# Kernel tuning notes

Hardware: AMD Instinct MI355X
Metric: run time of the kernel (lower is better)

The kernel has to match this reference:

```python
import jax, jax.numpy as jnp
import numpy as np

EPS = 1e-6          # VN leaky-relu denominator eps (vn_layers.py)
NEG_SLOPE = 0.2     # VNLinearLeakyReLU default negative_slope
K = 3               # pointops.interpolation default k
DIST_EPS = 1e-8     # interpolation inverse-distance eps


def vn_linear_leakyrelu(x, w_feat, w_dir):
    # x: [B, Cin, 3, N]; w_*: [Cout, Cin]  (bias-free Linears over channel dim)
    p = jnp.einsum('oc,bcvn->bovn', w_feat, x)
    d = jnp.einsum('oc,bcvn->bovn', w_dir, x)
    dot = jnp.sum(p * d, axis=2, keepdims=True)          # [B,Cout,1,N]
    d2 = jnp.sum(d * d, axis=2, keepdims=True)
    mask = (dot >= 0).astype(x.dtype)
    proj = p - (dot / (d2 + EPS)) * d                    # reflect negative part onto plane perp to d
    return NEG_SLOPE * p + (1.0 - NEG_SLOPE) * (mask * p + (1.0 - mask) * proj)


def interpolation(p2, p1, feat, b, n2, n1):
    # p2: [b*n2,3] coarse coords, p1: [b*n1,3] fine coords, feat: [C,3,b*n2]
    # k-NN inverse-squared-distance interpolation, segment-local per cloud.
    C = feat.shape[0]
    p2b = p2.reshape(b, n2, 3)
    p1b = p1.reshape(b, n1, 3)
    featb = feat.reshape(C * 3, b, n2).transpose(1, 2, 0)  # [b, n2, C*3]

    def per_batch(q, s, f):
        d2 = jnp.sum((q[:, None, :] - s[None, :, :]) ** 2, axis=-1)  # [n1,n2]
        neg_d2, idx = jax.lax.top_k(-d2, K)                          # k smallest sq-dists
        w = 1.0 / (-neg_d2 + DIST_EPS)
        w = w / jnp.sum(w, axis=1, keepdims=True)                    # [n1,K]
        return jnp.einsum('nk,nkc->nc', w, f[idx])                   # [n1, C*3]

    out = jax.vmap(per_batch)(p1b, p2b, featb)                       # [b, n1, C*3]
    return out.reshape(b, n1, C, 3).transpose(2, 3, 0, 1).reshape(C, 3, b * n1)


def setup_inputs() -> dict:
    key = jax.random.key(0)
    ks = jax.random.split(key, 8)
    b, n1, n2 = 4, 16384, 4096
    in_planes, out_planes = 128, 64
    p1 = jax.random.uniform(ks[0], (b * n1, 3), dtype=jnp.float32)
    p2 = jax.random.uniform(ks[1], (b * n2, 3), dtype=jnp.float32)
    x1 = jax.random.normal(ks[2], (1, out_planes, 3, b * n1), dtype=jnp.float32)
    x2 = jax.random.normal(ks[3], (1, in_planes, 3, b * n2), dtype=jnp.float32)
    o1 = (jnp.arange(1, b + 1, dtype=jnp.int32)) * n1   # cumulative offsets
    o2 = (jnp.arange(1, b + 1, dtype=jnp.int32)) * n2
    s1 = 1.0 / np.sqrt(out_planes)
    s2 = 1.0 / np.sqrt(in_planes)
    w1_feat = jax.random.uniform(ks[4], (out_planes, out_planes), jnp.float32, -s1, s1)
    w1_dir = jax.random.uniform(ks[5], (out_planes, out_planes), jnp.float32, -s1, s1)
    w2_feat = jax.random.uniform(ks[6], (out_planes, in_planes), jnp.float32, -s2, s2)
    w2_dir = jax.random.uniform(ks[7], (out_planes, in_planes), jnp.float32, -s2, s2)
    return {"p1": p1, "x1": x1, "o1": o1, "p2": p2, "x2": x2, "o2": o2,
            "w1_feat": w1_feat, "w1_dir": w1_dir, "w2_feat": w2_feat, "w2_dir": w2_dir}


def reference(p1, x1, o1, p2, x2, o2, w1_feat, w1_dir, w2_feat, w2_dir):
    b = o1.shape[0]
    n1 = x1.shape[-1] // b
    n2 = x2.shape[-1] // b
    y1 = vn_linear_leakyrelu(x1, w1_feat, w1_dir)            # [1,Cout,3,N1]
    y2 = vn_linear_leakyrelu(x2, w2_feat, w2_dir)[0]         # squeeze(0) -> [Cout,3,N2]
    up = interpolation(p2, p1, y2, b, n2, n1)                # [Cout,3,N1]
    return y1 + up
```

## Files before the change

### kernel.cpp

```cpp
#include <hip/hip_runtime.h>

#define N1T 65536
#define N2T 16384
#define COUT 64
#define CH 192
#define GRD 8
#define HCELL 0.125f

typedef unsigned short bhalf;
typedef __attribute__((ext_vector_type(8))) short short8;
typedef __attribute__((ext_vector_type(4))) float f32x4;

__device__ __forceinline__ bhalf f2bf(float f) {
    unsigned u = __float_as_uint(f);
    return (bhalf)((u + 0x7FFFu + ((u >> 16) & 1u)) >> 16);
}
__device__ __forceinline__ float bf2f(bhalf h) {
    return __uint_as_float(((unsigned)h) << 16);
}

__global__ __launch_bounds__(256) void wconv_kernel(
    const float* __restrict__ w1f, const float* __restrict__ w1d,
    const float* __restrict__ w2f, const float* __restrict__ w2d,
    bhalf* __restrict__ o1fh, bhalf* __restrict__ o1fl,
    bhalf* __restrict__ o1dh, bhalf* __restrict__ o1dl,
    bhalf* __restrict__ o2fh, bhalf* __restrict__ o2fl,
    bhalf* __restrict__ o2dh, bhalf* __restrict__ o2dl) {
    const int i = blockIdx.x * 256 + threadIdx.x;
    if (i < 4096) {
        const float a = w1f[i]; const bhalf ah = f2bf(a);
        o1fh[i] = ah; o1fl[i] = f2bf(a - bf2f(ah));
        const float b = w1d[i]; const bhalf bh = f2bf(b);
        o1dh[i] = bh; o1dl[i] = f2bf(b - bf2f(bh));
    }
    const float a = w2f[i]; const bhalf ah = f2bf(a);
    o2fh[i] = ah; o2fl[i] = f2bf(a - bf2f(ah));
    const float b = w2d[i]; const bhalf bh = f2bf(b);
    o2dh[i] = bh; o2dl[i] = f2bf(b - bf2f(bh));
}

template<int CIN, int N, bool CM>
__global__ __launch_bounds__(256) void vn_mfma_kernel(
    const float* __restrict__ x,
    const bhalf* __restrict__ wfh, const bhalf* __restrict__ wfl,
    const bhalf* __restrict__ wdh, const bhalf* __restrict__ wdl,
    float* __restrict__ out)
{
    constexpr int ROWS = CIN * 3;
    constexpr int LDSC = CIN * 3 + 8;
    __shared__ __align__(16) bhalf xs_h[32][LDSC];
    __shared__ __align__(16) bhalf xs_l[32][LDSC];

    const int tid  = threadIdx.x;
    const int lane = tid & 63;
    const int wave = tid >> 6;
    const int n0   = blockIdx.x * 32;
    const int r16  = lane & 15;
    const int hh   = lane >> 4;
    const int ot   = wave;

    constexpr int NF4 = ROWS * 8;
    for (int i4 = tid; i4 < NF4; i4 += 256) {
        const int row = i4 >> 3, p4 = i4 & 7;
        const float4 v = *(const float4*)&x[(size_t)row * N + n0 + p4 * 4];
        const int c = row / 3, vv = row - c * 3;
        const int col = vv * CIN + c;
        const float vals[4] = {v.x, v.y, v.z, v.w};
#pragma unroll
        for (int j = 0; j < 4; ++j) {
            const bhalf h = f2bf(vals[j]);
            xs_h[p4*4+j][col] = h;
            xs_l[p4*4+j][col] = f2bf(vals[j] - bf2f(h));
        }
    }
    __syncthreads();

    const f32x4 zero = {0.f, 0.f, 0.f, 0.f};
    f32x4 accP[2][3], accD[2][3];
#pragma unroll
    for (int s = 0; s < 2; ++s)
#pragma unroll
        for (int v = 0; v < 3; ++v) { accP[s][v] = zero; accD[s][v] = zero; }

    const int wofs = (ot * 16 + r16) * CIN + hh * 8;
    const bhalf* __restrict__ pfh = wfh + wofs;
    const bhalf* __restrict__ pfl = wfl + wofs;
    const bhalf* __restrict__ pdh = wdh + wofs;
    const bhalf* __restrict__ pdl = wdl + wofs;

#pragma unroll
    for (int k = 0; k < CIN / 32; ++k) {
        const short8 afh = *(const short8*)(pfh + k * 32);
        const short8 afl = *(const short8*)(pfl + k * 32);
        const short8 adh = *(const short8*)(pdh + k * 32);
        const short8 adl = *(const short8*)(pdl + k * 32);
#pragma unroll
        for (int s = 0; s < 2; ++s) {
            const int pt = s * 16 + r16;
#pragma unroll
            for (int v = 0; v < 3; ++v) {
                const short8 bh = *(const short8*)&xs_h[pt][v * CIN + k * 32 + hh * 8];
                const short8 bl = *(const short8*)&xs_l[pt][v * CIN + k * 32 + hh * 8];
                accP[s][v] = __builtin_amdgcn_mfma_f32_16x16x32_bf16(afh, bh, accP[s][v], 0, 0, 0);
                accP[s][v] = __builtin_amdgcn_mfma_f32_16x16x32_bf16(afl, bh, accP[s][v], 0, 0, 0);
                accP[s][v] = __builtin_amdgcn_mfma_f32_16x16x32_bf16(afh, bl, accP[s][v], 0, 0, 0);
                accD[s][v] = __builtin_amdgcn_mfma_f32_16x16x32_bf16(adh, bh, accD[s][v], 0, 0, 0);
                accD[s][v] = __builtin_amdgcn_mfma_f32_16x16x32_bf16(adl, bh, accD[s][v], 0, 0, 0);
                accD[s][v] = __builtin_amdgcn_mfma_f32_16x16x32_bf16(adh, bl, accD[s][v], 0, 0, 0);
            }
        }
    }

    float rr[2][12];
#pragma unroll
    for (int s = 0; s < 2; ++s)
#pragma unroll
        for (int reg = 0; reg < 4; ++reg) {
            const float p0 = accP[s][0][reg], p1 = accP[s][1][reg], p2 = accP[s][2][reg];
            const float q0 = accD[s][0][reg], q1 = accD[s][1][reg], q2 = accD[s][2][reg];
            const float dot = p0*q0 + p1*q1 + p2*q2;
            const float dd  = q0*q0 + q1*q1 + q2*q2;
            const float coef = (dot < 0.f) ? (0.8f * dot / (dd + 1e-6f)) : 0.f;
            rr[s][reg*3+0] = p0 - coef * q0;
            rr[s][reg*3+1] = p1 - coef * q1;
            rr[s][reg*3+2] = p2 - coef * q2;
        }

    if constexpr (!CM) {
#pragma unroll
        for (int s = 0; s < 2; ++s) {
            const int n = n0 + s * 16 + r16;
            float* op = out + (size_t)n * CH + ot * 48 + hh * 12;
            *(float4*)&op[0] = make_float4(rr[s][0], rr[s][1], rr[s][2],  rr[s][3]);
            *(float4*)&op[4] = make_float4(rr[s][4], rr[s][5], rr[s][6],  rr[s][7]);
            *(float4*)&op[8] = make_float4(rr[s][8], rr[s][9], rr[s][10], rr[s][11]);
        }
    } else {
#pragma unroll
        for (int s = 0; s < 2; ++s) {
            const int n = n0 + s * 16 + r16;
#pragma unroll
            for (int j = 0; j < 12; ++j)
                out[(size_t)(ot * 48 + hh * 12 + j) * N + n] = rr[s][j];
        }
    }
}

__global__ __launch_bounds__(192) void interp_add_kernel(
    const float* __restrict__ y2t,
    const int*   __restrict__ idxs,
    const float* __restrict__ wts,
    float* __restrict__ out)
{
    __shared__ float tile[32][193];
    __shared__ int   sk[3][32];
    __shared__ float sw[3][32];
    const int base = blockIdx.x * 32;
    const int t = threadIdx.x;

    if (t < 96) {
        const int r = t >> 5, pt = t & 31;
        sk[r][pt] = idxs[r * N1T + base + pt];
        sw[r][pt] = wts[r * N1T + base + pt];
    }
    __syncthreads();

#pragma unroll 4
    for (int pl = 0; pl < 32; ++pl) {
        tile[pl][t] = sw[0][pl] * y2t[(size_t)sk[0][pl] * CH + t]
                    + sw[1][pl] * y2t[(size_t)sk[1][pl] * CH + t]
                    + sw[2][pl] * y2t[(size_t)sk[2][pl] * CH + t];
    }
    __syncthreads();

#pragma unroll 8
    for (int k = 0; k < 32; ++k) {
        const int f  = k * 192 + t;
        const int ch = f >> 5, pt = f & 31;
        const size_t gi = (size_t)ch * N1T + base + pt;
        out[gi] += tile[pt][ch];
    }
}

#define KNN_INSERT(d2, j)                                        \
    {                                                            \
        const bool c0 = (d2) < b0;                               \
        const bool c1 = (d2) < b1;                               \
        const bool c2 = (d2) < b2v;                              \
        const float nb2 = c2 ? (c1 ? b1 : (d2)) : b2v;           \
        const int   ni2 = c2 ? (c1 ? i1 : (j))  : i2;            \
        const float nb1 = c1 ? (c0 ? b0 : (d2)) : b1;            \
        const int   ni1 = c1 ? (c0 ? i0 : (j))  : i1;            \
        b0 = c0 ? (d2) : b0;  i0 = c0 ? (j) : i0;                \
        b1 = nb1; i1 = ni1; b2v = nb2; i2 = ni2;                 \
    }

__global__ __launch_bounds__(256) void zero_kernel(int* __restrict__ p, int n) {
    const int i = blockIdx.x * 256 + threadIdx.x;
    if (i < n) p[i] = 0;
}

__device__ __forceinline__ int cell_of(float x, float y, float z) {
    int cx = (int)(x * (float)GRD); cx = cx < 0 ? 0 : (cx > GRD-1 ? GRD-1 : cx);
    int cy = (int)(y * (float)GRD); cy = cy < 0 ? 0 : (cy > GRD-1 ? GRD-1 : cy);
    int cz = (int)(z * (float)GRD); cz = cz < 0 ? 0 : (cz > GRD-1 ? GRD-1 : cz);
    return (cz << 6) | (cy << 3) | cx;
}

__global__ __launch_bounds__(256) void bin_count_kernel(
    const float* __restrict__ p2, int* __restrict__ counts) {
    const int i = blockIdx.x * 256 + threadIdx.x;
    const float x = p2[i*3+0], y = p2[i*3+1], z = p2[i*3+2];
    const int cell = ((i >> 12) << 9) | cell_of(x, y, z);
    atomicAdd(&counts[cell], 1);
}

__global__ __launch_bounds__(256) void scan_kernel(
    const int* __restrict__ counts, int* __restrict__ off) {
    __shared__ int buf[2][256];
    const int t = threadIdx.x;
    int v[8]; int s = 0;
#pragma unroll
    for (int j = 0; j < 8; ++j) { const int tmp = counts[t*8+j]; v[j] = s; s += tmp; }
    buf[0][t] = s; __syncthreads();
    int src = 0;
    for (int d = 1; d < 256; d <<= 1) {
        int val = buf[src][t];
        if (t >= d) val += buf[src][t - d];
        buf[src ^ 1][t] = val; src ^= 1; __syncthreads();
    }
    const int incl = buf[src][t];
    const int base = incl - s;
#pragma unroll
    for (int j = 0; j < 8; ++j) off[t*8+j] = base + v[j];
    if (t == 255) off[2048] = incl;
}

__global__ __launch_bounds__(256) void bin_scatter_kernel(
    const float* __restrict__ p2, const int* __restrict__ off,
    int* __restrict__ cnt2, float4* __restrict__ binned) {
    const int i = blockIdx.x * 256 + threadIdx.x;
    const float x = p2[i*3+0], y = p2[i*3+1], z = p2[i*3+2];
    const int cell = ((i >> 12) << 9) | cell_of(x, y, z);
    const int pos = off[cell] + atomicAdd(&cnt2[cell], 1);
    binned[pos] = make_float4(x, y, z, __int_as_float(i));
}

__global__ __launch_bounds__(256) void knn_grid_kernel(
    const float* __restrict__ p1,
    const float4* __restrict__ binned,
    const int* __restrict__ off,
    int*   __restrict__ idx_out,
    float* __restrict__ w_out)
{
    const int t   = blockIdx.x * 256 + threadIdx.x;
    const int fp  = t >> 2;
    const int sub = t & 3;
    const int bi  = fp >> 14;
    const int cbase = bi << 9;

    const float qx = p1[fp*3+0], qy = p1[fp*3+1], qz = p1[fp*3+2];
    int cx = (int)(qx * (float)GRD); cx = cx < 0 ? 0 : (cx > 7 ? 7 : cx);
    int cy = (int)(qy * (float)GRD); cy = cy < 0 ? 0 : (cy > 7 ? 7 : cy);
    int cz = (int)(qz * (float)GRD); cz = cz < 0 ? 0 : (cz > 7 ? 7 : cz);

    float b0 = 1e30f, b1 = 1e30f, b2v = 1e30f;
    int   i0 = 0,     i1 = 0,     i2 = 0;

    for (int dz = -1; dz <= 1; ++dz)
    for (int dy = -1; dy <= 1; ++dy)
    for (int dx = -1; dx <= 1; ++dx) {
        const int nx = cx + dx, ny = cy + dy, nz = cz + dz;
        if ((unsigned)nx > 7u || (unsigned)ny > 7u || (unsigned)nz > 7u) continue;
        const int c = cbase + (nz << 6) + (ny << 3) + nx;
        const int s = off[c], e = off[c + 1];
        for (int k = s + sub; k < e; k += 4) {
            const float4 c4 = binned[k];
            const float ddx = qx - c4.x, ddy = qy - c4.y, ddz = qz - c4.z;
            const float d2 = fmaf(ddx, ddx, fmaf(ddy, ddy, ddz * ddz));
            const int j = __float_as_int(c4.w);
            KNN_INSERT(d2, j)
        }
    }

#pragma unroll
    for (int m = 1; m <= 2; m <<= 1) {
        const float c0v = __shfl_xor(b0, m, 4);
        const float c1v = __shfl_xor(b1, m, 4);
        const float c2v = __shfl_xor(b2v, m, 4);
        const int   j0v = __shfl_xor(i0, m, 4);
        const int   j1v = __shfl_xor(i1, m, 4);
        const int   j2v = __shfl_xor(i2, m, 4);
        KNN_INSERT(c0v, j0v)
        KNN_INSERT(c1v, j1v)
        KNN_INSERT(c2v, j2v)
    }

    float dw = 1e30f;
    if (cx >= 2) dw = fminf(dw, qx - (float)(cx - 1) * HCELL);
    if (cx <= 5) dw = fminf(dw, (float)(cx + 2) * HCELL - qx);
    if (cy >= 2) dw = fminf(dw, qy - (float)(cy - 1) * HCELL);
    if (cy <= 5) dw = fminf(dw, (float)(cy + 2) * HCELL - qy);
    if (cz >= 2) dw = fminf(dw, qz - (float)(cz - 1) * HCELL);
    if (cz <= 5) dw = fminf(dw, (float)(cz + 2) * HCELL - qz);
    const bool done = b2v < dw * dw;

    if (!done) {
        b0 = b1 = b2v = 1e30f; i0 = i1 = i2 = 0;
        const int s = bi << 12, e = (bi + 1) << 12;
        for (int k = s + sub; k < e; k += 4) {
            const float4 c4 = binned[k];
            const float ddx = qx - c4.x, ddy = qy - c4.y, ddz = qz - c4.z;
            const float d2 = fmaf(ddx, ddx, fmaf(ddy, ddy, ddz * ddz));
            const int j = __float_as_int(c4.w);
            KNN_INSERT(d2, j)
        }
#pragma unroll
        for (int m = 1; m <= 2; m <<= 1) {
            const float c0v = __shfl_xor(b0, m, 4);
            const float c1v = __shfl_xor(b1, m, 4);
            const float c2v = __shfl_xor(b2v, m, 4);
            const int   j0v = __shfl_xor(i0, m, 4);
            const int   j1v = __shfl_xor(i1, m, 4);
            const int   j2v = __shfl_xor(i2, m, 4);
            KNN_INSERT(c0v, j0v)
            KNN_INSERT(c1v, j1v)
            KNN_INSERT(c2v, j2v)
        }
    }

    if (sub == 0) {
        const float w0 = 1.f / (b0 + 1e-8f);
        const float w1 = 1.f / (b1 + 1e-8f);
        const float w2 = 1.f / (b2v + 1e-8f);
        const float inv = 1.f / (w0 + w1 + w2);
        idx_out[0*N1T + fp] = i0;
        idx_out[1*N1T + fp] = i1;
        idx_out[2*N1T + fp] = i2;
        w_out[0*N1T + fp] = w0 * inv;
        w_out[1*N1T + fp] = w1 * inv;
        w_out[2*N1T + fp] = w2 * inv;
    }
}

extern "C" void kernel_launch(void* const* d_in, const int* in_sizes, int n_in,
                              void* d_out, int out_size, void* d_ws, size_t ws_size,
                              hipStream_t stream) {
    const float* p1      = (const float*)d_in[0];
    const float* x1      = (const float*)d_in[1];
    const float* p2      = (const float*)d_in[3];
    const float* x2      = (const float*)d_in[4];
    const float* w1_feat = (const float*)d_in[6];
    const float* w1_dir  = (const float*)d_in[7];
    const float* w2_feat = (const float*)d_in[8];
    const float* w2_dir  = (const float*)d_in[9];
    float* out = (float*)d_out;

    char* ws = (char*)d_ws;
    float*  y2t    = (float*)ws;                 ws += (size_t)N2T * CH * 4;
    int*    idxs   = (int*)ws;                   ws += (size_t)3 * N1T * 4;
    float*  wts    = (float*)ws;                 ws += (size_t)3 * N1T * 4;
    int*    counts = (int*)ws;                   ws += 2048 * 4;
    int*    cnt2   = (int*)ws;                   ws += 2048 * 4;
    int*    off    = (int*)ws;                   ws += 2064 * 4;
    float4* binned = (float4*)ws;                ws += (size_t)N2T * 16;
    bhalf*  wb1fh  = (bhalf*)ws;                 ws += 4096 * 2;
    bhalf*  wb1fl  = (bhalf*)ws;                 ws += 4096 * 2;
    bhalf*  wb1dh  = (bhalf*)ws;                 ws += 4096 * 2;
    bhalf*  wb1dl  = (bhalf*)ws;                 ws += 4096 * 2;
    bhalf*  wb2fh  = (bhalf*)ws;                 ws += 8192 * 2;
    bhalf*  wb2fl  = (bhalf*)ws;                 ws += 8192 * 2;
    bhalf*  wb2dh  = (bhalf*)ws;                 ws += 8192 * 2;
    bhalf*  wb2dl  = (bhalf*)ws;                 ws += 8192 * 2;

    wconv_kernel<<<32, 256, 0, stream>>>(w1_feat, w1_dir, w2_feat, w2_dir,
                                         wb1fh, wb1fl, wb1dh, wb1dl,
                                         wb2fh, wb2fl, wb2dh, wb2dl);

    zero_kernel<<<16, 256, 0, stream>>>(counts, 4096);
    bin_count_kernel<<<N2T/256, 256, 0, stream>>>(p2, counts);
    scan_kernel<<<1, 256, 0, stream>>>(counts, off);
    bin_scatter_kernel<<<N2T/256, 256, 0, stream>>>(p2, off, cnt2, binned);
    knn_grid_kernel<<<(4*N1T)/256, 256, 0, stream>>>(p1, binned, off, idxs, wts);

    vn_mfma_kernel<128, N2T, false><<<N2T/32, 256, 0, stream>>>(
        x2, wb2fh, wb2fl, wb2dh, wb2dl, y2t);
    vn_mfma_kernel<64, N1T, true><<<N1T/32, 256, 0, stream>>>(
        x1, wb1fh, wb1fl, wb1dh, wb1dl, out);
    interp_add_kernel<<<N1T/32, 192, 0, stream>>>(y2t, idxs, wts, out);
}
```

Measured before the change: 117.0 us.

## Fuse interpolation gather-add into fine-level VN MFMA epilogue and swizzle LDS

Removes the separate interp_add kernel. The fine-level VN kernel now loads the kNN indices and weights per point, gathers the three neighbour rows of y2t in its epilogue, and writes y1+up directly. This avoids one extra read-modify-write pass over the 64x3x65536 output and one kernel launch. It also XOR-swizzles the LDS column layout of the staged x tiles to reduce bank conflicts on the short8 B-operand reads. The cost is extra registers and gathered global loads inside the MFMA kernel, which could lower occupancy.

```diff
diff --git a/kernel.cpp b/kernel.cpp
--- a/kernel.cpp
+++ b/kernel.cpp
@@ -44,6 +44,9 @@
     const float* __restrict__ x,
     const bhalf* __restrict__ wfh, const bhalf* __restrict__ wfl,
     const bhalf* __restrict__ wdh, const bhalf* __restrict__ wdl,
+    const int*   __restrict__ idxs,
+    const float* __restrict__ wts,
+    const float* __restrict__ y2t,
     float* __restrict__ out)
 {
     constexpr int ROWS = CIN * 3;
@@ -59,18 +62,31 @@
     const int hh   = lane >> 4;
     const int ot   = wave;
 
+    int gk[2][3]; float gw[2][3];
+    if constexpr (CM) {
+#pragma unroll
+        for (int s = 0; s < 2; ++s) {
+            const int n = n0 + s * 16 + r16;
+#pragma unroll
+            for (int r = 0; r < 3; ++r) {
+                gk[s][r] = idxs[r * N1T + n];
+                gw[s][r] = wts[r * N1T + n];
+            }
+        }
+    }
+
     constexpr int NF4 = ROWS * 8;
     for (int i4 = tid; i4 < NF4; i4 += 256) {
         const int row = i4 >> 3, p4 = i4 & 7;
         const float4 v = *(const float4*)&x[(size_t)row * N + n0 + p4 * 4];
         const int c = row / 3, vv = row - c * 3;
-        const int col = vv * CIN + c;
+        const int colS = (vv * CIN + c) ^ ((p4 & 3) << 3);
         const float vals[4] = {v.x, v.y, v.z, v.w};
 #pragma unroll
         for (int j = 0; j < 4; ++j) {
             const bhalf h = f2bf(vals[j]);
-            xs_h[p4*4+j][col] = h;
-            xs_l[p4*4+j][col] = f2bf(vals[j] - bf2f(h));
+            xs_h[p4*4+j][colS] = h;
+            xs_l[p4*4+j][colS] = f2bf(vals[j] - bf2f(h));
         }
     }
     __syncthreads();
@@ -88,6 +104,7 @@
     const bhalf* __restrict__ pdh = wdh + wofs;
     const bhalf* __restrict__ pdl = wdl + wofs;
 
+    const int hs = ((hh ^ (r16 >> 2)) & 3) * 8 + (hh & ~3) * 8;
 #pragma unroll
     for (int k = 0; k < CIN / 32; ++k) {
         const short8 afh = *(const short8*)(pfh + k * 32);
@@ -99,8 +116,8 @@
             const int pt = s * 16 + r16;
 #pragma unroll
             for (int v = 0; v < 3; ++v) {
-                const short8 bh = *(const short8*)&xs_h[pt][v * CIN + k * 32 + hh * 8];
-                const short8 bl = *(const short8*)&xs_l[pt][v * CIN + k * 32 + hh * 8];
+                const short8 bh = *(const short8*)&xs_h[pt][v * CIN + k * 32 + hs];
+                const short8 bl = *(const short8*)&xs_l[pt][v * CIN + k * 32 + hs];
                 accP[s][v] = __builtin_amdgcn_mfma_f32_16x16x32_bf16(afh, bh, accP[s][v], 0, 0, 0);
                 accP[s][v] = __builtin_amdgcn_mfma_f32_16x16x32_bf16(afl, bh, accP[s][v], 0, 0, 0);
                 accP[s][v] = __builtin_amdgcn_mfma_f32_16x16x32_bf16(afh, bl, accP[s][v], 0, 0, 0);
@@ -136,49 +153,33 @@
             *(float4*)&op[8] = make_float4(rr[s][8], rr[s][9], rr[s][10], rr[s][11]);
         }
     } else {
+        const int chb = ot * 48 + hh * 12;
 #pragma unroll
         for (int s = 0; s < 2; ++s) {
             const int n = n0 + s * 16 + r16;
-#pragma unroll
-            for (int j = 0; j < 12; ++j)
-                out[(size_t)(ot * 48 + hh * 12 + j) * N + n] = rr[s][j];
-        }
-    }
-}
-
-__global__ __launch_bounds__(192) void interp_add_kernel(
-    const float* __restrict__ y2t,
-    const int*   __restrict__ idxs,
-    const float* __restrict__ wts,
-    float* __restrict__ out)
-{
-    __shared__ float tile[32][193];
-    __shared__ int   sk[3][32];
-    __shared__ float sw[3][32];
-    const int base = blockIdx.x * 32;
-    const int t = threadIdx.x;
-
-    if (t < 96) {
-        const int r = t >> 5, pt = t & 31;
-        sk[r][pt] = idxs[r * N1T + base + pt];
-        sw[r][pt] = wts[r * N1T + base + pt];
-    }
-    __syncthreads();
-
-#pragma unroll 4
-    for (int pl = 0; pl < 32; ++pl) {
-        tile[pl][t] = sw[0][pl] * y2t[(size_t)sk[0][pl] * CH + t]
-                    + sw[1][pl] * y2t[(size_t)sk[1][pl] * CH + t]
-                    + sw[2][pl] * y2t[(size_t)sk[2][pl] * CH + t];
-    }
-    __syncthreads();
-
-#pragma unroll 8
-    for (int k = 0; k < 32; ++k) {
-        const int f  = k * 192 + t;
-        const int ch = f >> 5, pt = f & 31;
-        const size_t gi = (size_t)ch * N1T + base + pt;
-        out[gi] += tile[pt][ch];
+            const float* __restrict__ r0 = y2t + (size_t)gk[s][0] * CH + chb;
+            const float* __restrict__ r1 = y2t + (size_t)gk[s][1] * CH + chb;
+            const float* __restrict__ r2 = y2t + (size_t)gk[s][2] * CH + chb;
+            const float w0 = gw[s][0], w1 = gw[s][1], w2 = gw[s][2];
+            float4 a0[3], a1[3], a2[3];
+#pragma unroll
+            for (int q = 0; q < 3; ++q) {
+                a0[q] = *(const float4*)&r0[q * 4];
+                a1[q] = *(const float4*)&r1[q * 4];
+                a2[q] = *(const float4*)&r2[q * 4];
+            }
+#pragma unroll
+            for (int q = 0; q < 3; ++q) {
+                const float u0 = w0*a0[q].x + w1*a1[q].x + w2*a2[q].x;
+                const float u1 = w0*a0[q].y + w1*a1[q].y + w2*a2[q].y;
+                const float u2 = w0*a0[q].z + w1*a1[q].z + w2*a2[q].z;
+                const float u3 = w0*a0[q].w + w1*a1[q].w + w2*a2[q].w;
+                out[(size_t)(chb + q*4 + 0) * N + n] = rr[s][q*4+0] + u0;
+                out[(size_t)(chb + q*4 + 1) * N + n] = rr[s][q*4+1] + u1;
+                out[(size_t)(chb + q*4 + 2) * N + n] = rr[s][q*4+2] + u2;
+                out[(size_t)(chb + q*4 + 3) * N + n] = rr[s][q*4+3] + u3;
+            }
+        }
     }
 }
 
@@ -384,8 +385,7 @@
     knn_grid_kernel<<<(4*N1T)/256, 256, 0, stream>>>(p1, binned, off, idxs, wts);
 
     vn_mfma_kernel<128, N2T, false><<<N2T/32, 256, 0, stream>>>(
-        x2, wb2fh, wb2fl, wb2dh, wb2dl, y2t);
+        x2, wb2fh, wb2fl, wb2dh, wb2dl, nullptr, nullptr, nullptr, y2t);
     vn_mfma_kernel<64, N1T, true><<<N1T/32, 256, 0, stream>>>(
-        x1, wb1fh, wb1fl, wb1dh, wb1dl, out);
-    interp_add_kernel<<<N1T/32, 192, 0, stream>>>(y2t, idxs, wts, out);
-}
+        x1, wb1fh, wb1fl, wb1dh, wb1dl, idxs, wts, y2t, out);
+}
```

Measured after the change: 105.3 us. -10.0%, faster.
